# Performance work log

Hardware: AMD Instinct MI355X
Metric: run time of the kernel (lower is better)

## Reference

```python
import jax, jax.numpy as jnp
import numpy as np

N = 50000      # nodes
E = 600000     # edges
B = 256        # graphs in batch
F_IN = 128     # num_features
H = 128        # nhid
D = 3 * H      # Set2Set in_channels (concat of 3 conv outputs)
C = 10         # num_classes
STEPS = 10     # Set2Set processing steps


def setup_inputs() -> dict:
    key = jax.random.key(0)
    ks = jax.random.split(key, 24)

    def gn(k, shape, fan_in):
        return jax.random.normal(k, shape, dtype=jnp.float32) / jnp.sqrt(jnp.float32(fan_in))

    x = jax.random.normal(ks[0], (N, F_IN), dtype=jnp.float32)
    edge_index = jax.random.randint(ks[1], (2, E), 0, N, dtype=jnp.int32)
    # sorted graph-assignment covering all B segments
    batch = (jnp.arange(N, dtype=jnp.int32) * B) // N

    inp = dict(x=x, edge_index=edge_index, batch=batch)
    # GraphConv params: out = x @ W_root + aggr(x_j) @ W_rel + b
    inp["W1_root"] = gn(ks[2], (F_IN, H), F_IN)
    inp["W1_rel"] = gn(ks[3], (F_IN, H), F_IN)
    inp["b1"] = jnp.zeros((H,), jnp.float32)
    inp["W2_root"] = gn(ks[4], (H, H), H)
    inp["W2_rel"] = gn(ks[5], (H, H), H)
    inp["b2"] = jnp.zeros((H,), jnp.float32)
    inp["W3_root"] = gn(ks[6], (H, H), H)
    inp["W3_rel"] = gn(ks[7], (H, H), H)
    inp["b3"] = jnp.zeros((H,), jnp.float32)
    # Set2Set LSTM: input 2*D, hidden D, gate order i,f,g,o
    inp["W_ih"] = gn(ks[8], (4 * D, 2 * D), 2 * D)
    inp["W_hh"] = gn(ks[9], (4 * D, D), D)
    inp["b_ih"] = jnp.zeros((4 * D,), jnp.float32)
    inp["b_hh"] = jnp.zeros((4 * D,), jnp.float32)
    # MLP head
    inp["lin1_W"] = gn(ks[10], (2 * D, H), 2 * D)
    inp["lin1_b"] = jnp.zeros((H,), jnp.float32)
    inp["lin2_W"] = gn(ks[11], (H, H // 2), H)
    inp["lin2_b"] = jnp.zeros((H // 2,), jnp.float32)
    inp["lin3_W"] = gn(ks[12], (H // 2, C), H // 2)
    inp["lin3_b"] = jnp.zeros((C,), jnp.float32)
    return inp


def _graph_conv(x, src, dst, W_root, W_rel, b):
    # sum_{j in N(i)} x_j, then linear; plus root transform
    agg = jax.ops.segment_sum(x[src], dst, num_segments=N)  # [N, F]
    return jax.nn.relu(x @ W_root + agg @ W_rel + b)


def _segment_softmax(e, seg, num):
    m = jax.ops.segment_max(e, seg, num_segments=num)
    ex = jnp.exp(e - m[seg])
    den = jax.ops.segment_sum(ex, seg, num_segments=num)
    return ex / den[seg]


def _set2set(x, batch, W_ih, W_hh, b_ih, b_hh):
    # x: [N, D], returns [B, 2D]
    q_star = jnp.zeros((B, 2 * D), x.dtype)
    h = jnp.zeros((B, D), x.dtype)
    c = jnp.zeros((B, D), x.dtype)
    for _ in range(STEPS):
        gates = q_star @ W_ih.T + b_ih + h @ W_hh.T + b_hh  # [B, 4D]
        i, f, g, o = jnp.split(gates, 4, axis=-1)
        i, f, o = jax.nn.sigmoid(i), jax.nn.sigmoid(f), jax.nn.sigmoid(o)
        c = f * c + i * jnp.tanh(g)
        h = o * jnp.tanh(c)
        q = h                                              # [B, D]
        e = jnp.sum(x * q[batch], axis=-1)                 # [N]
        a = _segment_softmax(e, batch, B)                  # [N]
        r = jax.ops.segment_sum(a[:, None] * x, batch, num_segments=B)  # [B, D]
        q_star = jnp.concatenate([q, r], axis=-1)
    return q_star


def reference(x, edge_index, batch,
              W1_root, W1_rel, b1, W2_root, W2_rel, b2, W3_root, W3_rel, b3,
              W_ih, W_hh, b_ih, b_hh,
              lin1_W, lin1_b, lin2_W, lin2_b, lin3_W, lin3_b):
    src, dst = edge_index[0], edge_index[1]
    x1 = _graph_conv(x, src, dst, W1_root, W1_rel, b1)
    x2 = _graph_conv(x1, src, dst, W2_root, W2_rel, b2)
    x3 = _graph_conv(x2, src, dst, W3_root, W3_rel, b3)
    xc = jnp.concatenate([x1, x2, x3], axis=1)             # [N, 3H]
    p = _set2set(xc, batch, W_ih, W_hh, b_ih, b_hh)        # [B, 6H]
    h1 = jax.nn.relu(p @ lin1_W + lin1_b)
    # dropout p=0.5 is identity in eval mode
    h2 = jax.nn.relu(h1 @ lin2_W + lin2_b)
    return jax.nn.log_softmax(h2 @ lin3_W + lin3_b, axis=-1)
```

## Files before the change

### kernel.cpp

```cpp
#include <hip/hip_runtime.h>
#include <hip/hip_bf16.h>
#include <cstddef>

constexpr int NN = 50000;
constexpr int EE = 600000;
constexpr int BBg = 256;

typedef __attribute__((ext_vector_type(8))) short short8;
typedef __attribute__((ext_vector_type(4))) float f32x4;

__device__ __forceinline__ unsigned short bf16_rne(float f) {
    unsigned int u = __float_as_uint(f);
    unsigned int r = u + 0x7fffu + ((u >> 16) & 1u);
    return (unsigned short)(r >> 16);
}
__device__ __forceinline__ float bf16_tof(unsigned short h) {
    return __uint_as_float(((unsigned int)h) << 16);
}

__global__ __launch_bounds__(256) void bake_bimg(
    const float* __restrict__ Wr1, const float* __restrict__ Wl1,
    const float* __restrict__ Wr2, const float* __restrict__ Wl2,
    const float* __restrict__ Wr3, const float* __restrict__ Wl3,
    unsigned short* __restrict__ bimg)
{
    int t = blockIdx.x * 256 + threadIdx.x;
    const int kp = t % 384;
    int rest = t / 384;
    const int c = rest & 63;  rest >>= 6;
    const int cb = rest & 3;  rest >>= 2;
    const int l = rest;
    const int kk = kp & 127;
    const int gc = cb * 64 + c;
    const float* W;
    if (gc < 128) W = (l == 0) ? Wr1 : (l == 1) ? Wr2 : Wr3;
    else          W = (l == 0) ? Wl1 : (l == 1) ? Wl2 : Wl3;
    const float v = W[kk * 128 + (gc & 127)];
    const unsigned short hi = bf16_rne(v);
    unsigned short out = hi;
    if (kp >= 256) out = bf16_rne(v - bf16_tof(hi));
    const int e = (c * 384 + kp) ^ ((c & 7) << 3);
    bimg[(l * 4 + cb) * 24576 + e] = out;
}

__global__ __launch_bounds__(256) void prep_x2(const float* __restrict__ x,
                                               unsigned short* __restrict__ x2)
{
    const int t = blockIdx.x * 256 + threadIdx.x;
    if (t >= NN * 128) return;
    const int n = t >> 7, k = t & 127;
    const float v = x[t];
    const unsigned short hi = bf16_rne(v);
    x2[(size_t)n * 256 + k] = hi;
    x2[(size_t)n * 256 + 128 + k] = bf16_rne(v - bf16_tof(hi));
}

__global__ __launch_bounds__(256) void conv_mfma(
    const unsigned short* __restrict__ x2,
    const unsigned short* __restrict__ bimg,
    float* __restrict__ tu,
    const float* __restrict__ bias)
{
    __shared__ unsigned short Bt[24576];
    const int tid = threadIdx.x;
    const int cb = blockIdx.x;
    const int rBase = blockIdx.y * 128;

    {
        const unsigned short* src = bimg + cb * 24576;
#pragma unroll
        for (int i = 0; i < 12; ++i) {
            const int e = (tid + i * 256) * 8;
            *(uint4*)&Bt[e] = *(const uint4*)&src[e];
        }
    }
    __syncthreads();

    const int lane = tid & 63;
    const int w = tid >> 6;
    const int r0w = rBase + w * 32;
    const int l15 = lane & 15;
    const int kg = lane >> 4;

    f32x4 acc[2][4];
#pragma unroll
    for (int rf = 0; rf < 2; ++rf)
#pragma unroll
        for (int cf = 0; cf < 4; ++cf) acc[rf][cf] = (f32x4){0.f, 0.f, 0.f, 0.f};

    const int rr0 = r0w + l15;
    const int rr1 = r0w + 16 + l15;
    const unsigned short* arow0 = x2 + (size_t)(rr0 < NN ? rr0 : NN - 1) * 256 + kg * 8;
    const unsigned short* arow1 = x2 + (size_t)(rr1 < NN ? rr1 : NN - 1) * 256 + kg * 8;

#pragma unroll
    for (int s = 0; s < 12; ++s) {
        const int acol = (s < 8 ? s : s - 8) * 32;
        const short8 a0 = *(const short8*)(arow0 + acol);
        const short8 a1 = *(const short8*)(arow1 + acol);
        short8 bfr[4];
#pragma unroll
        for (int cf = 0; cf < 4; ++cf) {
            const int c = cf * 16 + l15;
            const int e = (c * 384 + s * 32 + kg * 8) ^ ((c & 7) << 3);
            bfr[cf] = *(const short8*)&Bt[e];
        }
#pragma unroll
        for (int cf = 0; cf < 4; ++cf) {
            acc[0][cf] = __builtin_amdgcn_mfma_f32_16x16x32_bf16(a0, bfr[cf], acc[0][cf], 0, 0, 0);
            acc[1][cf] = __builtin_amdgcn_mfma_f32_16x16x32_bf16(a1, bfr[cf], acc[1][cf], 0, 0, 0);
        }
    }
    const int c0 = cb * 64;
#pragma unroll
    for (int rf = 0; rf < 2; ++rf) {
#pragma unroll
        for (int reg = 0; reg < 4; ++reg) {
            const int grow = r0w + rf * 16 + kg * 4 + reg;
            if (grow < NN) {
#pragma unroll
                for (int cf = 0; cf < 4; ++cf) {
                    const int gc = c0 + cf * 16 + l15;
                    float v = acc[rf][cf][reg];
                    if (gc < 128) v += bias[gc];
                    tu[(size_t)grow * 256 + gc] = v;
                }
            }
        }
    }
}

template<int TM>
__device__ __forceinline__ int swz(int k, int r) {
    return r ^ (((k >> 2) & (TM / 4 - 1)) << 2);
}

template<int RPT>
__global__ __launch_bounds__(256) void gemm_tile(
    const float* __restrict__ A, int lda,
    const float* __restrict__ B, int ldb,
    float* __restrict__ C, int ldc,
    int M, int Kper,
    const float* __restrict__ bias, int biasCols)
{
    constexpr int TM = RPT * 16;
    __shared__ float At[128][TM];
    __shared__ float Bs[128][64];
    const int tid = threadIdx.x;
    const int r0 = blockIdx.y * TM;
    const int c0 = blockIdx.x * 64;
    const int z = blockIdx.z;
    A += (size_t)z * Kper;
    B += (size_t)z * Kper * ldb;
    C += (size_t)z * (size_t)M * ldc;

    float acc[RPT][4];
#pragma unroll
    for (int i = 0; i < RPT; ++i)
#pragma unroll
        for (int j = 0; j < 4; ++j) acc[i][j] = 0.f;

    const int tc = (tid & 15) * 4;
    const int tr = (tid >> 4) * RPT;

    for (int kc = 0; kc < Kper; kc += 128) {
        {
            const int k4 = (tid & 31) * 4;
            const int rb = tid >> 5;
#pragma unroll
            for (int i = 0; i < TM / 8; ++i) {
                const int rr = rb + i * 8;
                const int grow = r0 + rr;
                float4 v = make_float4(0.f, 0.f, 0.f, 0.f);
                if (grow < M) v = *(const float4*)(A + (size_t)grow * lda + kc + k4);
                At[k4 + 0][swz<TM>(k4 + 0, rr)] = v.x;
                At[k4 + 1][swz<TM>(k4 + 1, rr)] = v.y;
                At[k4 + 2][swz<TM>(k4 + 2, rr)] = v.z;
                At[k4 + 3][swz<TM>(k4 + 3, rr)] = v.w;
            }
        }
        {
            const int c4 = (tid & 15) * 4;
            const int kb = tid >> 4;
#pragma unroll
            for (int i = 0; i < 8; ++i) {
                const int kk = kb + i * 16;
                float4 v = *(const float4*)(B + (size_t)(kc + kk) * ldb + c0 + c4);
                *(float4*)&Bs[kk][c4] = v;
            }
        }
        __syncthreads();
#pragma unroll 4
        for (int k = 0; k < 128; ++k) {
            float a[RPT];
            if constexpr (RPT == 4) {
                const float4 t4 = *(const float4*)&At[k][swz<TM>(k, tr)];
                a[0] = t4.x; a[1] = t4.y; a[2] = t4.z; a[3] = t4.w;
            } else {
                const float2 t2 = *(const float2*)&At[k][swz<TM>(k, tr)];
                a[0] = t2.x; a[1] = t2.y;
            }
            const float4 bv = *(const float4*)&Bs[k][tc];
#pragma unroll
            for (int i = 0; i < RPT; ++i) {
                acc[i][0] = fmaf(a[i], bv.x, acc[i][0]);
                acc[i][1] = fmaf(a[i], bv.y, acc[i][1]);
                acc[i][2] = fmaf(a[i], bv.z, acc[i][2]);
                acc[i][3] = fmaf(a[i], bv.w, acc[i][3]);
            }
        }
        __syncthreads();
    }
#pragma unroll
    for (int i = 0; i < RPT; ++i) {
        const int grow = r0 + tr + i;
        if (grow >= M) continue;
        const int gc = c0 + tc;
        float4 v = make_float4(acc[i][0], acc[i][1], acc[i][2], acc[i][3]);
        if (gc < biasCols) {
            v.x += bias[gc + 0]; v.y += bias[gc + 1];
            v.z += bias[gc + 2]; v.w += bias[gc + 3];
        }
        *(float4*)(C + (size_t)grow * ldc + gc) = v;
    }
}

__global__ __launch_bounds__(256) void deg_hist(const int* __restrict__ ei,
                                                int* __restrict__ deg)
{
    const int e = blockIdx.x * 256 + threadIdx.x;
    if (e < EE) atomicAdd(&deg[ei[EE + e]], 1);
}

__global__ __launch_bounds__(256) void scan1(const int* __restrict__ deg,
                                             int* __restrict__ tmp_ex,
                                             int* __restrict__ bsum)
{
    __shared__ int s[256];
    const int i = blockIdx.x * 256 + threadIdx.x;
    const int v = (i < NN) ? deg[i] : 0;
    s[threadIdx.x] = v;
    __syncthreads();
#pragma unroll
    for (int off = 1; off < 256; off <<= 1) {
        const int t = (threadIdx.x >= off) ? s[threadIdx.x - off] : 0;
        __syncthreads();
        s[threadIdx.x] += t;
        __syncthreads();
    }
    tmp_ex[i] = s[threadIdx.x] - v;
    if (threadIdx.x == 255) bsum[blockIdx.x] = s[255];
}

__global__ __launch_bounds__(256) void scan2(const int* __restrict__ bsum,
                                             int* __restrict__ boff)
{
    __shared__ int s[256];
    const int v = (threadIdx.x < 196) ? bsum[threadIdx.x] : 0;
    s[threadIdx.x] = v;
    __syncthreads();
#pragma unroll
    for (int off = 1; off < 256; off <<= 1) {
        const int t = (threadIdx.x >= off) ? s[threadIdx.x - off] : 0;
        __syncthreads();
        s[threadIdx.x] += t;
        __syncthreads();
    }
    if (threadIdx.x < 196) boff[threadIdx.x] = s[threadIdx.x] - v;
}

__global__ __launch_bounds__(256) void scan3(const int* __restrict__ tmp_ex,
                                             const int* __restrict__ boff,
                                             int* __restrict__ rowptr,
                                             int* __restrict__ cursor)
{
    const int i = blockIdx.x * 256 + threadIdx.x;
    if (i < NN) {
        const int r = tmp_ex[i] + boff[blockIdx.x];
        rowptr[i] = r;
        cursor[i] = r;
    }
    if (i == 0) rowptr[NN] = EE;
}

__global__ __launch_bounds__(256) void scatter_edges(const int* __restrict__ ei,
                                                     int* __restrict__ cursor,
                                                     int* __restrict__ col)
{
    const int e = blockIdx.x * 256 + threadIdx.x;
    if (e >= EE) return;
    const int slot = atomicAdd(&cursor[ei[EE + e]], 1);
    col[slot] = ei[e];
}

__global__ __launch_bounds__(256) void agg_relu(const int* __restrict__ rowptr,
                                                const int* __restrict__ col,
                                                const float* __restrict__ tu,
                                                float* __restrict__ xc, int coloff,
                                                unsigned short* __restrict__ x2n,
                                                int wsplit)
{
    const int node = blockIdx.x * 4 + (threadIdx.x >> 6);
    if (node >= NN) return;
    const int lane = threadIdx.x & 63;
    const int b = rowptr[node];
    const int e = rowptr[node + 1];
    const float* u = tu + 128 + lane * 2;

    float2 a0 = *(const float2*)&tu[(size_t)node * 256 + lane * 2];
    float2 a1 = make_float2(0.f, 0.f);
    float2 a2 = make_float2(0.f, 0.f);
    float2 a3 = make_float2(0.f, 0.f);

    int j = b;
    for (; j + 8 <= e; j += 8) {
        const int s0 = col[j + 0], s1 = col[j + 1], s2 = col[j + 2], s3 = col[j + 3];
        const int s4 = col[j + 4], s5 = col[j + 5], s6 = col[j + 6], s7 = col[j + 7];
        const float2 v0 = *(const float2*)(u + (size_t)s0 * 256);
        const float2 v1 = *(const float2*)(u + (size_t)s1 * 256);
        const float2 v2 = *(const float2*)(u + (size_t)s2 * 256);
        const float2 v3 = *(const float2*)(u + (size_t)s3 * 256);
        const float2 v4 = *(const float2*)(u + (size_t)s4 * 256);
        const float2 v5 = *(const float2*)(u + (size_t)s5 * 256);
        const float2 v6 = *(const float2*)(u + (size_t)s6 * 256);
        const float2 v7 = *(const float2*)(u + (size_t)s7 * 256);
        a0.x += v0.x; a0.y += v0.y;  a1.x += v1.x; a1.y += v1.y;
        a2.x += v2.x; a2.y += v2.y;  a3.x += v3.x; a3.y += v3.y;
        a0.x += v4.x; a0.y += v4.y;  a1.x += v5.x; a1.y += v5.y;
        a2.x += v6.x; a2.y += v6.y;  a3.x += v7.x; a3.y += v7.y;
    }
    for (; j < e; j += 4) {
        const bool c1 = (j + 1 < e), c2 = (j + 2 < e), c3 = (j + 3 < e);
        const int s0 = col[j];
        const int s1 = col[c1 ? j + 1 : j];
        const int s2 = col[c2 ? j + 2 : j];
        const int s3 = col[c3 ? j + 3 : j];
        const float2 v0 = *(const float2*)(u + (size_t)s0 * 256);
        const float2 v1 = *(const float2*)(u + (size_t)s1 * 256);
        const float2 v2 = *(const float2*)(u + (size_t)s2 * 256);
        const float2 v3 = *(const float2*)(u + (size_t)s3 * 256);
        a0.x += v0.x;              a0.y += v0.y;
        a1.x += c1 ? v1.x : 0.f;   a1.y += c1 ? v1.y : 0.f;
        a2.x += c2 ? v2.x : 0.f;   a2.y += c2 ? v2.y : 0.f;
        a3.x += c3 ? v3.x : 0.f;   a3.y += c3 ? v3.y : 0.f;
    }
    float2 acc;
    acc.x = (a0.x + a1.x) + (a2.x + a3.x);
    acc.y = (a0.y + a1.y) + (a2.y + a3.y);
    acc.x = fmaxf(acc.x, 0.f);
    acc.y = fmaxf(acc.y, 0.f);
    *(float2*)&xc[(size_t)node * 384 + coloff + lane * 2] = acc;

    if (wsplit) {
        const unsigned short h0 = bf16_rne(acc.x);
        const unsigned short h1 = bf16_rne(acc.y);
        const unsigned short l0 = bf16_rne(acc.x - bf16_tof(h0));
        const unsigned short l1 = bf16_rne(acc.y - bf16_tof(h1));
        unsigned short* p = x2n + (size_t)node * 256 + lane * 2;
        *(unsigned int*)p = (unsigned int)h0 | ((unsigned int)h1 << 16);
        *(unsigned int*)(p + 128) = (unsigned int)l0 | ((unsigned int)l1 << 16);
    }
}

__global__ __launch_bounds__(256) void build_wt(const float* __restrict__ w_ih,
                                                const float* __restrict__ w_hh,
                                                float* __restrict__ wt)
{
    const int t = blockIdx.x * 256 + threadIdx.x;
    const int k = t / 1536;
    const int j = t - k * 1536;
    float v = w_ih[(size_t)j * 768 + k];
    if (k < 384) v += w_hh[(size_t)j * 384 + k];
    wt[t] = v;
}

__global__ __launch_bounds__(512) void lstm_attn(const float* __restrict__ gpart,
                                                 const float* __restrict__ b_ih,
                                                 const float* __restrict__ b_hh,
                                                 float* __restrict__ cbuf,
                                                 float* __restrict__ qh,
                                                 const float* __restrict__ xc)
{
    const int b = blockIdx.x;
    const int start = (b * NN + BBg - 1) / BBg;
    const int end = ((b + 1) * NN + BBg - 1) / BBg;
    const int cnt = end - start;

    __shared__ float qs[384];
    __shared__ float wm[8], wz[8];
    __shared__ float rp[8][384];

    const int tid = threadIdx.x;
    const int lane = tid & 63;
    const int w = tid >> 6;

    if (tid < 384) {
        const int d = tid;
        const float* g0 = gpart + (size_t)b * 1536;
        const float* g1 = g0 + 256 * 1536;
        float gi = g0[d]        + g1[d]        + b_ih[d]        + b_hh[d];
        float gf = g0[384 + d]  + g1[384 + d]  + b_ih[384 + d]  + b_hh[384 + d];
        float gg = g0[768 + d]  + g1[768 + d]  + b_ih[768 + d]  + b_hh[768 + d];
        float go = g0[1152 + d] + g1[1152 + d] + b_ih[1152 + d] + b_hh[1152 + d];
        gi = 1.f / (1.f + expf(-gi));
        gf = 1.f / (1.f + expf(-gf));
        go = 1.f / (1.f + expf(-go));
        const float cc = gf * cbuf[b * 384 + d] + gi * tanhf(gg);
        cbuf[b * 384 + d] = cc;
        const float h = go * tanhf(cc);
        qh[(size_t)b * 768 + d] = h;
        qs[d] = h;
    }
    __syncthreads();

    float q[6];
#pragma unroll
    for (int j = 0; j < 6; ++j) q[j] = qs[lane + 64 * j];

    float m = -3.4e38f, Z = 0.f;
    float r[6] = {0.f, 0.f, 0.f, 0.f, 0.f, 0.f};
    for (int i = w; i < cnt; i += 8) {
        const float* xr = xc + (size_t)(start + i) * 384;
        float xv[6], d = 0.f;
#pragma unroll
        for (int j = 0; j < 6; ++j) { xv[j] = xr[lane + 64 * j]; d = fmaf(xv[j], q[j], d); }
#pragma unroll
        for (int s = 32; s > 0; s >>= 1) d += __shfl_xor(d, s);
        const float mn = fmaxf(m, d);
        const float cs = __expf(m - mn);
        const float p  = __expf(d - mn);
        Z = Z * cs + p;
#pragma unroll
        for (int j = 0; j < 6; ++j) r[j] = fmaf(r[j], cs, p * xv[j]);
        m = mn;
    }
#pragma unroll
    for (int j = 0; j < 6; ++j) rp[w][lane + 64 * j] = r[j];
    if (lane == 0) { wm[w] = m; wz[w] = Z; }
    __syncthreads();

    float M = wm[0];
#pragma unroll
    for (int i = 1; i < 8; ++i) M = fmaxf(M, wm[i]);
    float sc[8];
    float Zt = 0.f;
#pragma unroll
    for (int i = 0; i < 8; ++i) { sc[i] = __expf(wm[i] - M); Zt += wz[i] * sc[i]; }
    const float invZ = 1.f / Zt;
    for (int t = tid; t < 384; t += 512) {
        float rr = 0.f;
#pragma unroll
        for (int i2 = 0; i2 < 8; ++i2) rr = fmaf(rp[i2][t], sc[i2], rr);
        qh[(size_t)b * 768 + 384 + t] = rr * invZ;
    }
}

__global__ __launch_bounds__(128) void head1(const float* __restrict__ qh,
                                             const float* __restrict__ W,
                                             const float* __restrict__ bias,
                                             float* __restrict__ h1)
{
    const int b = blockIdx.x;
    const int tid = threadIdx.x;
    __shared__ float qs[768];
    for (int k = tid; k < 768; k += 128) qs[k] = qh[(size_t)b * 768 + k];
    __syncthreads();
    float acc = bias[tid];
    for (int k = 0; k < 768; ++k) acc = fmaf(qs[k], W[k * 128 + tid], acc);
    h1[b * 128 + tid] = fmaxf(acc, 0.f);
}

__global__ __launch_bounds__(64) void head2(const float* __restrict__ h1,
                                            const float* __restrict__ W2,
                                            const float* __restrict__ b2,
                                            const float* __restrict__ W3,
                                            const float* __restrict__ b3,
                                            float* __restrict__ out)
{
    const int b = blockIdx.x;
    const int tid = threadIdx.x;
    __shared__ float hs[128];
    __shared__ float h2s[64];
    __shared__ float lg[10];
    for (int k = tid; k < 128; k += 64) hs[k] = h1[b * 128 + k];
    __syncthreads();
    float acc = b2[tid];
    for (int k = 0; k < 128; ++k) acc = fmaf(hs[k], W2[k * 64 + tid], acc);
    h2s[tid] = fmaxf(acc, 0.f);
    __syncthreads();
    if (tid < 10) {
        float a = b3[tid];
        for (int k = 0; k < 64; ++k) a = fmaf(h2s[k], W3[k * 10 + tid], a);
        lg[tid] = a;
    }
    __syncthreads();
    if (tid < 10) {
        float m = lg[0];
        for (int j = 1; j < 10; ++j) m = fmaxf(m, lg[j]);
        float s = 0.f;
        for (int j = 0; j < 10; ++j) s += expf(lg[j] - m);
        out[b * 10 + tid] = lg[tid] - m - logf(s);
    }
}

extern "C" void kernel_launch(void* const* d_in, const int* in_sizes, int n_in,
                              void* d_out, int out_size, void* d_ws, size_t ws_size,
                              hipStream_t stream)
{
    const float* x     = (const float*)d_in[0];
    const int*   ei    = (const int*)d_in[1];
    const float* W1r   = (const float*)d_in[3];
    const float* W1l   = (const float*)d_in[4];
    const float* b1    = (const float*)d_in[5];
    const float* W2r   = (const float*)d_in[6];
    const float* W2l   = (const float*)d_in[7];
    const float* b2    = (const float*)d_in[8];
    const float* W3r   = (const float*)d_in[9];
    const float* W3l   = (const float*)d_in[10];
    const float* b3    = (const float*)d_in[11];
    const float* W_ih  = (const float*)d_in[12];
    const float* W_hh  = (const float*)d_in[13];
    const float* b_ih  = (const float*)d_in[14];
    const float* b_hh  = (const float*)d_in[15];
    const float* lin1W = (const float*)d_in[16];
    const float* lin1b = (const float*)d_in[17];
    const float* lin2W = (const float*)d_in[18];
    const float* lin2b = (const float*)d_in[19];
    const float* lin3W = (const float*)d_in[20];
    const float* lin3b = (const float*)d_in[21];

    float* ws = (float*)d_ws;
    float* xc    = ws;
    float* tu    = ws + 19200000;
    float* wt    = ws + 32000000;
    float* qh    = ws + 33179648;
    float* cbuf  = ws + 33376256;
    float* gpart = ws + 33474560;
    float* h1    = ws + 34260992;
    unsigned short* bimg = (unsigned short*)(ws + 34293760);
    unsigned short* x2   = (unsigned short*)(ws + 34441216);
    int*   ib    = (int*)(ws + 40841216);
    int* deg     = ib;
    int* rowptr  = ib + 50000;
    int* cursor  = ib + 100001;
    int* tmp_ex  = ib + 150001;
    int* bsum    = ib + 200177;
    int* boff    = ib + 200433;
    int* col     = ib + 200689;
    float* out   = (float*)d_out;

    hipMemsetAsync(qh, 0, (196608 + 98304) * sizeof(float), stream);
    hipMemsetAsync(deg, 0, 50000 * sizeof(int), stream);

    build_wt<<<4608, 256, 0, stream>>>(W_ih, W_hh, wt);
    bake_bimg<<<1152, 256, 0, stream>>>(W1r, W1l, W2r, W2l, W3r, W3l, bimg);
    prep_x2<<<25000, 256, 0, stream>>>(x, x2);

    deg_hist<<<2344, 256, 0, stream>>>(ei, deg);
    scan1<<<196, 256, 0, stream>>>(deg, tmp_ex, bsum);
    scan2<<<1, 256, 0, stream>>>(bsum, boff);
    scan3<<<196, 256, 0, stream>>>(tmp_ex, boff, rowptr, cursor);
    scatter_edges<<<2344, 256, 0, stream>>>(ei, cursor, col);

    const float* biases[3] = {b1, b2, b3};
    for (int l = 0; l < 3; ++l) {
        conv_mfma<<<dim3(4, 391), 256, 0, stream>>>(
            x2, bimg + l * 4 * 24576, tu, biases[l]);
        agg_relu<<<12500, 256, 0, stream>>>(rowptr, col, tu, xc, l * 128,
                                            x2, (l < 2) ? 1 : 0);
    }

    for (int s = 0; s < 10; ++s) {
        gemm_tile<2><<<dim3(24, 8, 2), 256, 0, stream>>>(
            qh, 768, wt, 1536, gpart, 1536, 256, 384, nullptr, 0);
        lstm_attn<<<256, 512, 0, stream>>>(gpart, b_ih, b_hh, cbuf, qh, xc);
    }

    head1<<<256, 128, 0, stream>>>(qh, lin1W, lin1b, h1);
    head2<<<256, 64, 0, stream>>>(h1, lin2W, lin2b, lin3W, lin3b, out);
}
```

Before: 842.5 us.

## Replace Set2Set gate FP32 GEMM with split-bf16 MFMA and widen attention blocks

The per-step LSTM gate GEMM moves from a tiled FP32 FMA kernel with split-K partials to an MFMA kernel. It uses a three-pass hi/lo bf16 split (hi*hi, lo*hi, hi*lo) to keep near-FP32 accuracy. The weights are pre-baked into a bf16 hi/lo MFMA layout, and lstm_attn now writes the split bf16 copy of q_star and reads a single gate buffer instead of summing two partials. lstm_attn also grows to 1024 threads (16 waves) to parallelise the per-graph attention reduction, and the Set2Set buffers reuse the dead tu region. The split-bf16 scheme drops the lo*lo term, which slightly changes numerics.

```diff
diff --git a/kernel.cpp b/kernel.cpp
--- a/kernel.cpp
+++ b/kernel.cpp
@@ -55,6 +55,23 @@
     x2[(size_t)n * 256 + 128 + k] = bf16_rne(v - bf16_tof(hi));
 }
 
+__global__ __launch_bounds__(256) void bake_wt2(const float* __restrict__ w_ih,
+                                                const float* __restrict__ w_hh,
+                                                unsigned short* __restrict__ wt2)
+{
+    const int t = blockIdx.x * 256 + threadIdx.x;
+    const int o = t & 7;
+    const int j = (t >> 3) % 1536;
+    const int rest = (t >> 3) / 1536;
+    const int kg = rest % 96;
+    const int v = rest / 96;
+    const int k = kg * 8 + o;
+    float val = w_ih[(size_t)j * 768 + k];
+    if (k < 384) val += w_hh[(size_t)j * 384 + k];
+    const unsigned short hi = bf16_rne(val);
+    wt2[t] = v ? bf16_rne(val - bf16_tof(hi)) : hi;
+}
+
 __global__ __launch_bounds__(256) void conv_mfma(
     const unsigned short* __restrict__ x2,
     const unsigned short* __restrict__ bimg,
@@ -130,99 +147,54 @@
     }
 }
 
-template<int TM>
-__device__ __forceinline__ int swz(int k, int r) {
-    return r ^ (((k >> 2) & (TM / 4 - 1)) << 2);
-}
-
-template<int RPT>
-__global__ __launch_bounds__(256) void gemm_tile(
-    const float* __restrict__ A, int lda,
-    const float* __restrict__ B, int ldb,
-    float* __restrict__ C, int ldc,
-    int M, int Kper,
-    const float* __restrict__ bias, int biasCols)
-{
-    constexpr int TM = RPT * 16;
-    __shared__ float At[128][TM];
-    __shared__ float Bs[128][64];
+__global__ __launch_bounds__(256) void gates_mfma(
+    const unsigned short* __restrict__ qh2,
+    const unsigned short* __restrict__ wt2,
+    float* __restrict__ gates)
+{
     const int tid = threadIdx.x;
-    const int r0 = blockIdx.y * TM;
+    const int lane = tid & 63;
+    const int w = tid >> 6;
     const int c0 = blockIdx.x * 64;
-    const int z = blockIdx.z;
-    A += (size_t)z * Kper;
-    B += (size_t)z * Kper * ldb;
-    C += (size_t)z * (size_t)M * ldc;
-
-    float acc[RPT][4];
-#pragma unroll
-    for (int i = 0; i < RPT; ++i)
-#pragma unroll
-        for (int j = 0; j < 4; ++j) acc[i][j] = 0.f;
-
-    const int tc = (tid & 15) * 4;
-    const int tr = (tid >> 4) * RPT;
-
-    for (int kc = 0; kc < Kper; kc += 128) {
-        {
-            const int k4 = (tid & 31) * 4;
-            const int rb = tid >> 5;
-#pragma unroll
-            for (int i = 0; i < TM / 8; ++i) {
-                const int rr = rb + i * 8;
-                const int grow = r0 + rr;
-                float4 v = make_float4(0.f, 0.f, 0.f, 0.f);
-                if (grow < M) v = *(const float4*)(A + (size_t)grow * lda + kc + k4);
-                At[k4 + 0][swz<TM>(k4 + 0, rr)] = v.x;
-                At[k4 + 1][swz<TM>(k4 + 1, rr)] = v.y;
-                At[k4 + 2][swz<TM>(k4 + 2, rr)] = v.z;
-                At[k4 + 3][swz<TM>(k4 + 3, rr)] = v.w;
+    const int r0w = blockIdx.y * 128 + w * 32;
+    const int l15 = lane & 15;
+    const int kg = lane >> 4;
+
+    f32x4 acc[2][4];
+#pragma unroll
+    for (int rf = 0; rf < 2; ++rf)
+#pragma unroll
+        for (int cf = 0; cf < 4; ++cf) acc[rf][cf] = (f32x4){0.f, 0.f, 0.f, 0.f};
+
+    const unsigned short* arow0 = qh2 + (size_t)(r0w + l15) * 1536 + kg * 8;
+    const unsigned short* arow1 = arow0 + 16 * 1536;
+
+#pragma unroll
+    for (int p = 0; p < 3; ++p) {
+        const int abase = (p == 1) ? 768 : 0;
+        const unsigned short* bbase = wt2 + (p == 2 ? 1179648 : 0)
+                                    + (size_t)(kg * 1536 + c0 + l15) * 8;
+#pragma unroll 4
+        for (int km = 0; km < 24; ++km) {
+            const short8 a0 = *(const short8*)(arow0 + abase + km * 32);
+            const short8 a1 = *(const short8*)(arow1 + abase + km * 32);
+#pragma unroll
+            for (int cf = 0; cf < 4; ++cf) {
+                const short8 bf = *(const short8*)(bbase + (size_t)km * 4 * 1536 * 8 + cf * 128);
+                acc[0][cf] = __builtin_amdgcn_mfma_f32_16x16x32_bf16(a0, bf, acc[0][cf], 0, 0, 0);
+                acc[1][cf] = __builtin_amdgcn_mfma_f32_16x16x32_bf16(a1, bf, acc[1][cf], 0, 0, 0);
             }
         }
-        {
-            const int c4 = (tid & 15) * 4;
-            const int kb = tid >> 4;
-#pragma unroll
-            for (int i = 0; i < 8; ++i) {
-                const int kk = kb + i * 16;
-                float4 v = *(const float4*)(B + (size_t)(kc + kk) * ldb + c0 + c4);
-                *(float4*)&Bs[kk][c4] = v;
-            }
+    }
+#pragma unroll
+    for (int rf = 0; rf < 2; ++rf)
+#pragma unroll
+        for (int reg = 0; reg < 4; ++reg) {
+            const int grow = r0w + rf * 16 + kg * 4 + reg;
+#pragma unroll
+            for (int cf = 0; cf < 4; ++cf)
+                gates[(size_t)grow * 1536 + c0 + cf * 16 + l15] = acc[rf][cf][reg];
         }
-        __syncthreads();
-#pragma unroll 4
-        for (int k = 0; k < 128; ++k) {
-            float a[RPT];
-            if constexpr (RPT == 4) {
-                const float4 t4 = *(const float4*)&At[k][swz<TM>(k, tr)];
-                a[0] = t4.x; a[1] = t4.y; a[2] = t4.z; a[3] = t4.w;
-            } else {
-                const float2 t2 = *(const float2*)&At[k][swz<TM>(k, tr)];
-                a[0] = t2.x; a[1] = t2.y;
-            }
-            const float4 bv = *(const float4*)&Bs[k][tc];
-#pragma unroll
-            for (int i = 0; i < RPT; ++i) {
-                acc[i][0] = fmaf(a[i], bv.x, acc[i][0]);
-                acc[i][1] = fmaf(a[i], bv.y, acc[i][1]);
-                acc[i][2] = fmaf(a[i], bv.z, acc[i][2]);
-                acc[i][3] = fmaf(a[i], bv.w, acc[i][3]);
-            }
-        }
-        __syncthreads();
-    }
-#pragma unroll
-    for (int i = 0; i < RPT; ++i) {
-        const int grow = r0 + tr + i;
-        if (grow >= M) continue;
-        const int gc = c0 + tc;
-        float4 v = make_float4(acc[i][0], acc[i][1], acc[i][2], acc[i][3]);
-        if (gc < biasCols) {
-            v.x += bias[gc + 0]; v.y += bias[gc + 1];
-            v.z += bias[gc + 2]; v.w += bias[gc + 3];
-        }
-        *(float4*)(C + (size_t)grow * ldc + gc) = v;
-    }
 }
 
 __global__ __launch_bounds__(256) void deg_hist(const int* __restrict__ ei,
@@ -362,24 +334,13 @@
     }
 }
 
-__global__ __launch_bounds__(256) void build_wt(const float* __restrict__ w_ih,
-                                                const float* __restrict__ w_hh,
-                                                float* __restrict__ wt)
-{
-    const int t = blockIdx.x * 256 + threadIdx.x;
-    const int k = t / 1536;
-    const int j = t - k * 1536;
-    float v = w_ih[(size_t)j * 768 + k];
-    if (k < 384) v += w_hh[(size_t)j * 384 + k];
-    wt[t] = v;
-}
-
-__global__ __launch_bounds__(512) void lstm_attn(const float* __restrict__ gpart,
-                                                 const float* __restrict__ b_ih,
-                                                 const float* __restrict__ b_hh,
-                                                 float* __restrict__ cbuf,
-                                                 float* __restrict__ qh,
-                                                 const float* __restrict__ xc)
+__global__ __launch_bounds__(1024) void lstm_attn(const float* __restrict__ gates,
+                                                  const float* __restrict__ b_ih,
+                                                  const float* __restrict__ b_hh,
+                                                  float* __restrict__ cbuf,
+                                                  float* __restrict__ qh,
+                                                  unsigned short* __restrict__ qh2,
+                                                  const float* __restrict__ xc)
 {
     const int b = blockIdx.x;
     const int start = (b * NN + BBg - 1) / BBg;
@@ -387,8 +348,8 @@
     const int cnt = end - start;
 
     __shared__ float qs[384];
-    __shared__ float wm[8], wz[8];
-    __shared__ float rp[8][384];
+    __shared__ float wm[16], wz[16];
+    __shared__ float rp[16][384];
 
     const int tid = threadIdx.x;
     const int lane = tid & 63;
@@ -396,12 +357,11 @@
 
     if (tid < 384) {
         const int d = tid;
-        const float* g0 = gpart + (size_t)b * 1536;
-        const float* g1 = g0 + 256 * 1536;
-        float gi = g0[d]        + g1[d]        + b_ih[d]        + b_hh[d];
-        float gf = g0[384 + d]  + g1[384 + d]  + b_ih[384 + d]  + b_hh[384 + d];
-        float gg = g0[768 + d]  + g1[768 + d]  + b_ih[768 + d]  + b_hh[768 + d];
-        float go = g0[1152 + d] + g1[1152 + d] + b_ih[1152 + d] + b_hh[1152 + d];
+        const float* g0 = gates + (size_t)b * 1536;
+        float gi = g0[d]        + b_ih[d]        + b_hh[d];
+        float gf = g0[384 + d]  + b_ih[384 + d]  + b_hh[384 + d];
+        float gg = g0[768 + d]  + b_ih[768 + d]  + b_hh[768 + d];
+        float go = g0[1152 + d] + b_ih[1152 + d] + b_hh[1152 + d];
         gi = 1.f / (1.f + expf(-gi));
         gf = 1.f / (1.f + expf(-gf));
         go = 1.f / (1.f + expf(-go));
@@ -410,6 +370,9 @@
         const float h = go * tanhf(cc);
         qh[(size_t)b * 768 + d] = h;
         qs[d] = h;
+        const unsigned short hi = bf16_rne(h);
+        qh2[(size_t)b * 1536 + d] = hi;
+        qh2[(size_t)b * 1536 + 768 + d] = bf16_rne(h - bf16_tof(hi));
     }
     __syncthreads();
 
@@ -419,7 +382,7 @@
 
     float m = -3.4e38f, Z = 0.f;
     float r[6] = {0.f, 0.f, 0.f, 0.f, 0.f, 0.f};
-    for (int i = w; i < cnt; i += 8) {
+    for (int i = w; i < cnt; i += 16) {
         const float* xr = xc + (size_t)(start + i) * 384;
         float xv[6], d = 0.f;
 #pragma unroll
@@ -441,17 +404,21 @@
 
     float M = wm[0];
 #pragma unroll
-    for (int i = 1; i < 8; ++i) M = fmaxf(M, wm[i]);
-    float sc[8];
+    for (int i = 1; i < 16; ++i) M = fmaxf(M, wm[i]);
+    float sc[16];
     float Zt = 0.f;
 #pragma unroll
-    for (int i = 0; i < 8; ++i) { sc[i] = __expf(wm[i] - M); Zt += wz[i] * sc[i]; }
+    for (int i = 0; i < 16; ++i) { sc[i] = __expf(wm[i] - M); Zt += wz[i] * sc[i]; }
     const float invZ = 1.f / Zt;
-    for (int t = tid; t < 384; t += 512) {
+    for (int t = tid; t < 384; t += 1024) {
         float rr = 0.f;
 #pragma unroll
-        for (int i2 = 0; i2 < 8; ++i2) rr = fmaf(rp[i2][t], sc[i2], rr);
-        qh[(size_t)b * 768 + 384 + t] = rr * invZ;
+        for (int i2 = 0; i2 < 16; ++i2) rr = fmaf(rp[i2][t], sc[i2], rr);
+        const float val = rr * invZ;
+        qh[(size_t)b * 768 + 384 + t] = val;
+        const unsigned short hi = bf16_rne(val);
+        qh2[(size_t)b * 1536 + 384 + t] = hi;
+        qh2[(size_t)b * 1536 + 1152 + t] = bf16_rne(val - bf16_tof(hi));
     }
 }
 
@@ -532,14 +499,15 @@
     float* ws = (float*)d_ws;
     float* xc    = ws;
     float* tu    = ws + 19200000;
-    float* wt    = ws + 32000000;
-    float* qh    = ws + 33179648;
-    float* cbuf  = ws + 33376256;
-    float* gpart = ws + 33474560;
-    float* h1    = ws + 34260992;
-    unsigned short* bimg = (unsigned short*)(ws + 34293760);
-    unsigned short* x2   = (unsigned short*)(ws + 34441216);
-    int*   ib    = (int*)(ws + 40841216);
+    float* qh    = tu;
+    float* cbuf  = tu + 196608;
+    float* gates = tu + 294912;
+    unsigned short* qh2 = (unsigned short*)(tu + 688128);
+    float* h1    = tu + 884736;
+    unsigned short* wt2  = (unsigned short*)(ws + 32000000);
+    unsigned short* bimg = (unsigned short*)(ws + 33179648);
+    unsigned short* x2   = (unsigned short*)(ws + 33327104);
+    int*   ib    = (int*)(ws + 39727104);
     int* deg     = ib;
     int* rowptr  = ib + 50000;
     int* cursor  = ib + 100001;
@@ -549,10 +517,9 @@
     int* col     = ib + 200689;
     float* out   = (float*)d_out;
 
-    hipMemsetAsync(qh, 0, (196608 + 98304) * sizeof(float), stream);
     hipMemsetAsync(deg, 0, 50000 * sizeof(int), stream);
 
-    build_wt<<<4608, 256, 0, stream>>>(W_ih, W_hh, wt);
+    bake_wt2<<<9216, 256, 0, stream>>>(W_ih, W_hh, wt2);
     bake_bimg<<<1152, 256, 0, stream>>>(W1r, W1l, W2r, W2l, W3r, W3l, bimg);
     prep_x2<<<25000, 256, 0, stream>>>(x, x2);
 
@@ -570,10 +537,12 @@
                                             x2, (l < 2) ? 1 : 0);
     }
 
+    hipMemsetAsync(qh, 0, (196608 + 98304) * sizeof(float), stream);
+    hipMemsetAsync(qh2, 0, 393216 * sizeof(unsigned short), stream);
+
     for (int s = 0; s < 10; ++s) {
-        gemm_tile<2><<<dim3(24, 8, 2), 256, 0, stream>>>(
-            qh, 768, wt, 1536, gpart, 1536, 256, 384, nullptr, 0);
-        lstm_attn<<<256, 512, 0, stream>>>(gpart, b_ih, b_hh, cbuf, qh, xc);
+        gates_mfma<<<dim3(24, 2), 256, 0, stream>>>(qh2, wt2, gates);
+        lstm_attn<<<256, 1024, 0, stream>>>(gates, b_ih, b_hh, cbuf, qh, qh2, xc);
     }
 
     head1<<<256, 128, 0, stream>>>(qh, lin1W, lin1b, h1);
```

Result: slower. 1.015 ms (+20.5%).
